# Performance work log

Measured on AMD Instinct MI355X. Metric: run time of the kernel, lower is better.

Reference implementation:

```python
import jax, jax.numpy as jnp
import numpy as np

LEN = 2048

def setup_inputs() -> dict:
    key = jax.random.key(0)
    k1, k2 = jax.random.split(key)
    x = jax.random.normal(k1, (LEN,), dtype=jnp.float32)
    y = jax.random.normal(k2, (LEN,), dtype=jnp.float32)
    return {"x": x, "y": y}

def reference(x, y):
    # Classic DTW DP with squared-difference cost.
    # Original torch code clamps indices with max(i-1,0)/max(j-1,0); because
    # DTW[i,j] is still +inf when read, the clamped reads reduce to the
    # standard recurrence: row 0 is a cumulative sum, col 0 uses only 'up',
    # interior uses min(up, left, diag).
    inf = jnp.float32(jnp.inf)
    cost0 = (x[0] - y) ** 2            # [len2]
    row0 = jnp.cumsum(cost0)           # DTW row i=0

    def row_step(prev_row, xi):
        cost = (xi - y) ** 2                                   # [len2]
        diag = jnp.concatenate([prev_row[:1], prev_row[:-1]])  # prev_row[j-1], clamped at j=0
        def cell(left, cud):
            c, up, dg = cud
            v = c + jnp.minimum(jnp.minimum(up, left), dg)
            return v, v
        # left init = inf => at j=0 min reduces to min(up, diag) = prev_row[0]
        _, new_row = jax.lax.scan(cell, inf, (cost, prev_row, diag))
        return new_row, None

    last_row, _ = jax.lax.scan(row_step, row0, x[1:])
    return jnp.sqrt(last_row[-1])
```

## Files before the change

kernel.cpp:

```cpp
#include <hip/hip_runtime.h>
#include <math.h>


#define NLEN  2048
#define NW    4
#define CSTEP 64
#define DSKEW 128
#define PAD   64
#define RROW  (PAD + 2112)
#define GTOT  2496
#define INFV  1e30f

__device__ __forceinline__ float dpp_shr1(float v, float inj) {
    int r = __builtin_amdgcn_update_dpp(
        __builtin_bit_cast(int, inj), __builtin_bit_cast(int, v),
        0x138 , 0xF, 0xF, false );
    return __builtin_bit_cast(float, r);
}
__device__ __forceinline__ float rdlane(float v, int l) {
    return __builtin_bit_cast(float,
        __builtin_amdgcn_readlane(__builtin_bit_cast(int, v), l));
}
__device__ __forceinline__ float min3f(float a, float b, float c) {
    return fminf(fminf(a, b), c);
}

__global__ __launch_bounds__(256, 1) void dtw_kernel(const float* __restrict__ X,
                                                     const float* __restrict__ Y,
                                                     float* __restrict__ out) {
    __shared__ __align__(16) float yS[NLEN];
    __shared__ float ring[(NW + 1) * RROW];

    const int tid  = threadIdx.x;
    const int w    = tid >> 6;
    const int lane = tid & 63;

    {
        const float4* Y4 = (const float4*)Y;
        float4* y4 = (float4*)yS;
        y4[tid]       = Y4[tid];
        y4[tid + 256] = Y4[tid + 256];
    }
    for (int k = tid; k < (NW + 1) * RROW; k += 256) ring[k] = INFV;
    __syncthreads();

    float x0, x1, x2, x3, x4, x5, x6, x7;
    {
        const float4 xa = *(const float4*)&X[tid * 8];
        const float4 xb = *(const float4*)&X[tid * 8 + 4];
        x0 = xa.x; x1 = xa.y; x2 = xa.z; x3 = xa.w;
        x4 = xb.x; x5 = xb.y; x6 = xb.z; x7 = xb.w;
    }

    float v0 = INFV, v1 = INFV, v2 = INFV, v3 = INFV;
    float v4 = INFV, v5 = INFV, v6 = INFV, v7 = INFV;
    float uprev = (tid == 0) ? 0.0f : INFV;
    float yconv = 0.0f;

    const float* ringR = ring + w * RROW + PAD;
    float*       ringW = ring + (w + 1) * RROW + PAD;

    for (int gb = 0; gb < GTOT; gb += CSTEP) {
        const int tau0 = gb - w * DSKEW;

        if (tau0 >= 0 && tau0 <= NLEN) {
            int yi = tau0 + lane;
            if (yi >= NLEN) yi = NLEN - 1;
            const float yblk = yS[yi];
            const float rblk = ringR[tau0 + lane];
            float* wp = ringW + (tau0 - lane);
            const bool isout = (tau0 == NLEN) & (w == NW - 1) & (lane == 63);

            #pragma unroll
            for (int s = 0; s < CSTEP; ++s) {
                const float yu = rdlane(yblk, s);
                const float ru = rdlane(rblk, s);
                yconv = dpp_shr1(yconv, yu);
                const float u = dpp_shr1(v7, ru);
                float d0 = x0 - yconv; float nv0 = fmaf(d0, d0, min3f(v0, uprev, u));
                float d1 = x1 - yconv; float nv1 = fmaf(d1, d1, min3f(v1, v0, nv0));
                float d2 = x2 - yconv; float nv2 = fmaf(d2, d2, min3f(v2, v1, nv1));
                float d3 = x3 - yconv; float nv3 = fmaf(d3, d3, min3f(v3, v2, nv2));
                float d4 = x4 - yconv; float nv4 = fmaf(d4, d4, min3f(v4, v3, nv3));
                float d5 = x5 - yconv; float nv5 = fmaf(d5, d5, min3f(v5, v4, nv4));
                float d6 = x6 - yconv; float nv6 = fmaf(d6, d6, min3f(v6, v5, nv5));
                float d7 = x7 - yconv; float nv7 = fmaf(d7, d7, min3f(v7, v6, nv6));
                wp[s] = nv7;
                uprev = u;
                v0 = nv0; v1 = nv1; v2 = nv2; v3 = nv3;
                v4 = nv4; v5 = nv5; v6 = nv6; v7 = nv7;
                if (s == 62 && isout) out[0] = sqrtf(nv7);
            }
        }
        __syncthreads();
    }
}

extern "C" void kernel_launch(void* const* d_in, const int* in_sizes, int n_in,
                              void* d_out, int out_size, void* d_ws, size_t ws_size,
                              hipStream_t stream) {
    const float* x = (const float*)d_in[0];
    const float* y = (const float*)d_in[1];
    (void)in_sizes; (void)n_in; (void)out_size; (void)d_ws; (void)ws_size;
    dtw_kernel<<<1, 256, 0, stream>>>(x, y, (float*)d_out);
}
```

Baseline: 198.0 us.

## Skew each thread's 8 rows into two half-pipelines to shorten per-step dependency chain

Splits each thread's 8-row column chain into two halves that work on different anti-diagonal steps: rows 4-7 use the previous step's y value and the stored v3 from the prior step, while rows 0-3 use the current y. The dependent min/fma chain per step shrinks from 8 to 4 links and the two halves can interleave. In exchange the lane-to-lane skew becomes 2 steps per lane, so the wavefront skew, ring padding, total step count and output timing are all enlarged, adding pipeline fill and drain steps.

```diff
diff --git a/kernel.cpp b/kernel.cpp
--- a/kernel.cpp
+++ b/kernel.cpp
@@ -5,10 +5,11 @@
 #define NLEN  2048
 #define NW    4
 #define CSTEP 64
-#define DSKEW 128
-#define PAD   64
-#define RROW  (PAD + 2112)
-#define GTOT  2496
+#define DSKEW 192
+#define PAD   128
+#define RROW  (PAD + 2176)
+#define GTOT  2752
+#define TAUMAX 2112
 #define INFV  1e30f
 
 __device__ __forceinline__ float dpp_shr1(float v, float inj) {
@@ -54,8 +55,9 @@
 
     float v0 = INFV, v1 = INFV, v2 = INFV, v3 = INFV;
     float v4 = INFV, v5 = INFV, v6 = INFV, v7 = INFV;
+    float v3m1 = INFV;
     float uprev = (tid == 0) ? 0.0f : INFV;
-    float yconv = 0.0f;
+    float yP = 0.0f, yQ = 0.0f, ym = 0.0f;
 
     const float* ringR = ring + w * RROW + PAD;
     float*       ringW = ring + (w + 1) * RROW + PAD;
@@ -63,33 +65,39 @@
     for (int gb = 0; gb < GTOT; gb += CSTEP) {
         const int tau0 = gb - w * DSKEW;
 
-        if (tau0 >= 0 && tau0 <= NLEN) {
+        if (tau0 >= 0 && tau0 <= TAUMAX) {
             int yi = tau0 + lane;
-            if (yi >= NLEN) yi = NLEN - 1;
+            if (yi > NLEN - 1) yi = NLEN - 1;
             const float yblk = yS[yi];
             const float rblk = ringR[tau0 + lane];
-            float* wp = ringW + (tau0 - lane);
-            const bool isout = (tau0 == NLEN) & (w == NW - 1) & (lane == 63);
+            float* wp = ringW + (tau0 - 2 * lane - 1);
+            const bool isout = (tau0 == TAUMAX) & (w == NW - 1) & (lane == 63);
 
             #pragma unroll
             for (int s = 0; s < CSTEP; ++s) {
-                const float yu = rdlane(yblk, s);
                 const float ru = rdlane(rblk, s);
-                yconv = dpp_shr1(yconv, yu);
-                const float u = dpp_shr1(v7, ru);
-                float d0 = x0 - yconv; float nv0 = fmaf(d0, d0, min3f(v0, uprev, u));
-                float d1 = x1 - yconv; float nv1 = fmaf(d1, d1, min3f(v1, v0, nv0));
-                float d2 = x2 - yconv; float nv2 = fmaf(d2, d2, min3f(v2, v1, nv1));
-                float d3 = x3 - yconv; float nv3 = fmaf(d3, d3, min3f(v3, v2, nv2));
-                float d4 = x4 - yconv; float nv4 = fmaf(d4, d4, min3f(v4, v3, nv3));
-                float d5 = x5 - yconv; float nv5 = fmaf(d5, d5, min3f(v5, v4, nv4));
-                float d6 = x6 - yconv; float nv6 = fmaf(d6, d6, min3f(v6, v5, nv5));
-                float d7 = x7 - yconv; float nv7 = fmaf(d7, d7, min3f(v7, v6, nv6));
+                if ((s & 1) == 0) {
+                    ym = yQ;
+                    yP = dpp_shr1(yP, rdlane(yblk, s));
+                    yQ = dpp_shr1(yQ, rdlane(yblk, s + 1));
+                }
+                const float yA = ((s & 1) == 0) ? yP : yQ;
+                const float yB = ((s & 1) == 0) ? ym : yP;
+                const float u  = dpp_shr1(v7, ru);
+                float d4 = x4 - yB; float nv4 = fmaf(d4, d4, min3f(v4, v3m1, v3));
+                float d5 = x5 - yB; float nv5 = fmaf(d5, d5, min3f(v5, v4, nv4));
+                float d6 = x6 - yB; float nv6 = fmaf(d6, d6, min3f(v6, v5, nv5));
+                float d7 = x7 - yB; float nv7 = fmaf(d7, d7, min3f(v7, v6, nv6));
+                float d0 = x0 - yA; float nv0 = fmaf(d0, d0, min3f(v0, uprev, u));
+                float d1 = x1 - yA; float nv1 = fmaf(d1, d1, min3f(v1, v0, nv0));
+                float d2 = x2 - yA; float nv2 = fmaf(d2, d2, min3f(v2, v1, nv1));
+                float d3 = x3 - yA; float nv3 = fmaf(d3, d3, min3f(v3, v2, nv2));
                 wp[s] = nv7;
-                uprev = u;
+                if (s == 62 && isout) out[0] = sqrtf(nv7);
+                v3m1 = v3;
                 v0 = nv0; v1 = nv1; v2 = nv2; v3 = nv3;
                 v4 = nv4; v5 = nv5; v6 = nv6; v7 = nv7;
-                if (s == 62 && isout) out[0] = sqrtf(nv7);
+                uprev = u;
             }
         }
         __syncthreads();
```

Measured after the change: 211.0 us. 1.07x slower.

## Double wavefronts to 8 with 4 rows per lane and circular LDS ring

Applied to the files above, without the earlier changes.

Splits the DTW wavefront across 8 wavefronts of 512 threads, each lane holding 4 rows of x instead of 8. The serial dependency chain per column step shrinks from 8 to 4 cells. Inter-wave rows now pass through a 256-entry circular ring buffer in LDS addressed with a mask, replacing full-length padded rows. In exchange the pipeline fill and drain grows, giving more outer steps and block barriers, and there are more cross-wave handoffs.

```diff
diff --git a/kernel.cpp b/kernel.cpp
--- a/kernel.cpp
+++ b/kernel.cpp
@@ -3,12 +3,11 @@
 
 
 #define NLEN  2048
-#define NW    4
+#define NW    8
 #define CSTEP 64
 #define DSKEW 128
-#define PAD   64
-#define RROW  (PAD + 2112)
-#define GTOT  2496
+#define RB    256
+#define GTOT  3008
 #define INFV  1e30f
 
 __device__ __forceinline__ float dpp_shr1(float v, float inj) {
@@ -25,71 +24,60 @@
     return fminf(fminf(a, b), c);
 }
 
-__global__ __launch_bounds__(256, 1) void dtw_kernel(const float* __restrict__ X,
+__global__ __launch_bounds__(512, 1) void dtw_kernel(const float* __restrict__ X,
                                                      const float* __restrict__ Y,
                                                      float* __restrict__ out) {
     __shared__ __align__(16) float yS[NLEN];
-    __shared__ float ring[(NW + 1) * RROW];
+    __shared__ float ring[(NW + 1) * RB];
 
     const int tid  = threadIdx.x;
     const int w    = tid >> 6;
     const int lane = tid & 63;
 
     {
-        const float4* Y4 = (const float4*)Y;
-        float4* y4 = (float4*)yS;
-        y4[tid]       = Y4[tid];
-        y4[tid + 256] = Y4[tid + 256];
+        ((float4*)yS)[tid] = ((const float4*)Y)[tid];
     }
-    for (int k = tid; k < (NW + 1) * RROW; k += 256) ring[k] = INFV;
+    for (int k = tid; k < (NW + 1) * RB; k += 512) ring[k] = INFV;
     __syncthreads();
 
-    float x0, x1, x2, x3, x4, x5, x6, x7;
+    float x0, x1, x2, x3;
     {
-        const float4 xa = *(const float4*)&X[tid * 8];
-        const float4 xb = *(const float4*)&X[tid * 8 + 4];
+        const float4 xa = *(const float4*)&X[tid * 4];
         x0 = xa.x; x1 = xa.y; x2 = xa.z; x3 = xa.w;
-        x4 = xb.x; x5 = xb.y; x6 = xb.z; x7 = xb.w;
     }
 
     float v0 = INFV, v1 = INFV, v2 = INFV, v3 = INFV;
-    float v4 = INFV, v5 = INFV, v6 = INFV, v7 = INFV;
     float uprev = (tid == 0) ? 0.0f : INFV;
     float yconv = 0.0f;
 
-    const float* ringR = ring + w * RROW + PAD;
-    float*       ringW = ring + (w + 1) * RROW + PAD;
+    const float* ringR = ring + w * RB;
+    float*       ringW = ring + (w + 1) * RB;
 
     for (int gb = 0; gb < GTOT; gb += CSTEP) {
         const int tau0 = gb - w * DSKEW;
 
         if (tau0 >= 0 && tau0 <= NLEN) {
             int yi = tau0 + lane;
-            if (yi >= NLEN) yi = NLEN - 1;
+            if (yi > NLEN - 1) yi = NLEN - 1;
             const float yblk = yS[yi];
-            const float rblk = ringR[tau0 + lane];
-            float* wp = ringW + (tau0 - lane);
-            const bool isout = (tau0 == NLEN) & (w == NW - 1) & (lane == 63);
+            const float rblk = ringR[(unsigned)(tau0 + lane) & (RB - 1u)];
+            const int   wb   = tau0 - lane;
+            const bool  isout = (tau0 == NLEN) & (w == NW - 1) & (lane == 63);
 
             #pragma unroll
             for (int s = 0; s < CSTEP; ++s) {
                 const float yu = rdlane(yblk, s);
                 const float ru = rdlane(rblk, s);
                 yconv = dpp_shr1(yconv, yu);
-                const float u = dpp_shr1(v7, ru);
+                const float u = dpp_shr1(v3, ru);
                 float d0 = x0 - yconv; float nv0 = fmaf(d0, d0, min3f(v0, uprev, u));
                 float d1 = x1 - yconv; float nv1 = fmaf(d1, d1, min3f(v1, v0, nv0));
                 float d2 = x2 - yconv; float nv2 = fmaf(d2, d2, min3f(v2, v1, nv1));
                 float d3 = x3 - yconv; float nv3 = fmaf(d3, d3, min3f(v3, v2, nv2));
-                float d4 = x4 - yconv; float nv4 = fmaf(d4, d4, min3f(v4, v3, nv3));
-                float d5 = x5 - yconv; float nv5 = fmaf(d5, d5, min3f(v5, v4, nv4));
-                float d6 = x6 - yconv; float nv6 = fmaf(d6, d6, min3f(v6, v5, nv5));
-                float d7 = x7 - yconv; float nv7 = fmaf(d7, d7, min3f(v7, v6, nv6));
-                wp[s] = nv7;
+                ringW[(unsigned)(wb + s) & (RB - 1u)] = nv3;
                 uprev = u;
                 v0 = nv0; v1 = nv1; v2 = nv2; v3 = nv3;
-                v4 = nv4; v5 = nv5; v6 = nv6; v7 = nv7;
-                if (s == 62 && isout) out[0] = sqrtf(nv7);
+                if (s == 62 && isout) out[0] = sqrtf(nv3);
             }
         }
         __syncthreads();
@@ -102,5 +90,5 @@
     const float* x = (const float*)d_in[0];
     const float* y = (const float*)d_in[1];
     (void)in_sizes; (void)n_in; (void)out_size; (void)d_ws; (void)ws_size;
-    dtw_kernel<<<1, 256, 0, stream>>>(x, y, (float*)d_out);
+    dtw_kernel<<<1, 512, 0, stream>>>(x, y, (float*)d_out);
 }
```

Measured after the change: 234.6 us. 18.4% more time.
